# Kernel optimization log

Measured on AMD Instinct MI355X. Metric: run time of the kernel, lower is better.

Reference implementation:

```python
import jax, jax.numpy as jnp
import numpy as np
from jax import lax

B, T, N, F_IN = 4, 12, 2048, 26
HID, LF, FF, HOR, K = 128, 32, 256, 12, 2
E = 16384
N_TEMPORAL = 3
ALPHA, BETA = 0.9, 0.8   # synaptic / membrane decay constants
EPS = 1e-5
CH = [HID + LF, HID + 2 * LF]  # per-block channel sizes: 160, 192


def setup_inputs() -> dict:
    key = jax.random.key(0)
    ks = iter(jax.random.split(key, 64))
    def nrm(shape, s=0.02):
        return jax.random.normal(next(ks), shape, jnp.float32) * s
    inp = {
        "x": jax.random.normal(next(ks), (B, T, N, F_IN), jnp.float32),
        "edge_index": jax.random.randint(next(ks), (2, E), 0, N),
        "edge_weight": jax.random.uniform(next(ks), (E,), jnp.float32),
        "enc_w": nrm((F_IN, HID)), "enc_b": jnp.zeros((HID,), jnp.float32),
        "node_emb": nrm((N, HID)),
        "src_emb": nrm((N, HID), 0.1), "tgt_emb": nrm((N, HID), 0.1),
    }
    for i, c in enumerate(CH):
        inp[f"lw{i}"] = nrm((N, LF))
        inp[f"tW{i}"] = nrm((N_TEMPORAL, c, c))
        inp[f"tb{i}"] = jnp.zeros((N_TEMPORAL, c), jnp.float32)
        inp[f"dcw{i}"] = nrm((2 * K * c, c)); inp[f"dcb{i}"] = jnp.zeros((c,), jnp.float32)
        inp[f"dsw{i}"] = nrm((2 * c, c));     inp[f"dsb{i}"] = jnp.zeros((c,), jnp.float32)
        inp[f"skw{i}"] = nrm((c, FF));        inp[f"skb{i}"] = jnp.zeros((FF,), jnp.float32)
        inp[f"ng{i}"] = jnp.ones((c,), jnp.float32)
        inp[f"nb{i}"] = jnp.zeros((c,), jnp.float32)
    inp["rw1"] = nrm((FF, 2 * FF)); inp["rb1"] = jnp.zeros((2 * FF,), jnp.float32)
    inp["rw2"] = nrm((2 * FF, HOR * F_IN)); inp["rb2"] = jnp.zeros((HOR * F_IN,), jnp.float32)
    return inp


def _prop(x, s, d, w):
    """One diffusion step: gather x at source nodes, weight, scatter-add to dest. x:[b,t,n,c]."""
    m = x[:, :, s, :] * w[None, None, :, None]          # [b,t,E,c]
    m = jnp.moveaxis(m, 2, 0)                            # [E,b,t,c]
    y = jax.ops.segment_sum(m, d, num_segments=N)        # [n,b,t,c]
    return jnp.moveaxis(y, 0, 2)


def _synaptic_chain(h, Ws, bs):
    """n_layers of Linear + synaptic (2nd-order LIF) temporal recurrence; returns full sequence."""
    def step(carry, inp):
        syn, mem = carry
        syn = ALPHA * syn + inp
        mem = BETA * mem + syn
        return (syn, mem), mem
    for l in range(Ws.shape[0]):
        ht = jnp.moveaxis(h @ Ws[l] + bs[l], 1, 0)       # [t,b,n,c]
        z = jnp.zeros_like(ht[0])
        _, out = lax.scan(step, (z, z), ht)
        h = jnp.moveaxis(out, 0, 1)
    return h


def _diffconv(x, src, dst, ew, W, b):
    """Order-K diffusion conv over forward + backward transition matrices."""
    deg_f = jax.ops.segment_sum(ew, dst, num_segments=N)
    w_f = ew / jnp.clip(deg_f[dst], 1e-6)
    deg_b = jax.ops.segment_sum(ew, src, num_segments=N)
    w_b = ew / jnp.clip(deg_b[src], 1e-6)
    outs = []
    z = x
    for _ in range(K):
        z = _prop(z, src, dst, w_f); outs.append(z)
    z = x
    for _ in range(K):
        z = _prop(z, dst, src, w_b); outs.append(z)
    return jnp.concatenate(outs, -1) @ W + b


def _dense_conv(x, adj, W, b):
    """Dense graph conv order 2, include_self=False: concat[A x, A^2 x] -> Linear."""
    x1 = jnp.einsum('wv,btvc->btwc', adj, x)
    x2 = jnp.einsum('wv,btvc->btwc', adj, x1)
    return jnp.concatenate([x1, x2], -1) @ W + b


def _batch_norm(x, g, b):
    mu = x.mean((0, 1, 2))
    var = x.var((0, 1, 2))
    return (x - mu) / jnp.sqrt(var + EPS) * g + b


def reference(x, edge_index, edge_weight, enc_w, enc_b, node_emb, src_emb, tgt_emb,
              lw0, tW0, tb0, dcw0, dcb0, dsw0, dsb0, skw0, skb0, ng0, nb0,
              lw1, tW1, tb1, dcw1, dcb1, dsw1, dsb1, skw1, skb1, ng1, nb1,
              rw1, rb1, rw2, rb2):
    src, dst = edge_index[0], edge_index[1]
    h = x @ enc_w + enc_b + node_emb                     # encoder + node embedding
    adj = jax.nn.softmax(jax.nn.relu(src_emb @ tgt_emb.T), axis=1)  # learned adjacency
    out = jnp.zeros((1, h.shape[1], 1, 1), h.dtype)
    blocks = [(lw0, tW0, tb0, dcw0, dcb0, dsw0, dsb0, skw0, skb0, ng0, nb0),
              (lw1, tW1, tb1, dcw1, dcb1, dsw1, dsb1, skw1, skb1, ng1, nb1)]
    for (lw, tW, tb, dcw, dcb, dsw, dsb, skw, skb, ng, nb) in blocks:
        lwB = jnp.broadcast_to(lw, (h.shape[0], h.shape[1]) + lw.shape)
        h = jnp.concatenate([h, lwB], -1)                # LearnableWeight: append learned features
        res = h
        h = _synaptic_chain(h, tW, tb)                   # temporal chain (membrane potential)
        out = h @ skw + skb + out[:, -h.shape[1]:]       # skip connection accumulator
        xs = _diffconv(h, src, dst, edge_weight, dcw, dcb)
        h = xs + _dense_conv(h, adj, dsw, dsb)
        h = h + res[:, -h.shape[1]:]
        h = _batch_norm(h, ng, nb)
    r = jax.nn.relu(out[:, -1])                          # readout on last step: [B,N,FF]
    r = jax.nn.relu(r @ rw1 + rb1)
    y = r @ rw2 + rb2                                    # [B,N,HOR*F_IN]
    return y.reshape(B, N, HOR, F_IN).transpose(0, 2, 1, 3)  # [B,HOR,N,F_IN]
```

## Files before the change

### kernel.cpp

```cpp
#include <hip/hip_runtime.h>

using u16 = unsigned short;
typedef short bf16x8 __attribute__((ext_vector_type(8)));
typedef float f32x4  __attribute__((ext_vector_type(4)));

__device__ __forceinline__ float bf2f(u16 u) { return __uint_as_float(((unsigned)u) << 16); }
__device__ __forceinline__ u16 f2bf(float f) {
  unsigned u = __float_as_uint(f);
  return (u16)((u + 0x7FFFu + ((u >> 16) & 1u)) >> 16);
}
__device__ __forceinline__ float ldv(const float* p) { return *p; }
__device__ __forceinline__ float ldv(const u16* p)   { return bf2f(*p); }
__device__ __forceinline__ void  stv(float* p, float v) { *p = v; }
__device__ __forceinline__ void  stv(u16* p, float v)   { *p = f2bf(v); }

constexpr int cB = 4, cT = 12, cN = 2048, cF = 26;
constexpr int cHID = 128, cLF = 32, cFF = 256, cHOR = 12;
constexpr int cE = 16384;
constexpr int cR = cB * cT * cN;
constexpr int cBT = cB * cT;
constexpr float cALPHA = 0.9f, cBETA = 0.8f, cEPS = 1e-5f;

#define FLAG_ACC  1
#define FLAG_BIAS 2
#define FLAG_RELU 4

template <int NF, typename TC>
__global__ __launch_bounds__(256)
void gemm_mfma(const u16* __restrict__ A, const u16* __restrict__ BT,
               TC* __restrict__ C, const float* __restrict__ bias,
               int M, int N, int K, int lda, int ldbt, int ldc,
               long batchA, long batchB, long batchC, int flags, int biasPerT)
{
  constexpr int TN = NF * 32;
  constexpr int ROWS = 128 + TN;
  constexpr int NINST = ROWS / 16;
  constexpr int NPW = (NINST + 3) / 4;
  __shared__ __align__(16) u16 S[2][ROWS * 32];

  const long gx = gridDim.x, gy = gridDim.y;
  const long total = gx * gy * (long)gridDim.z;
  long lid = blockIdx.x + gx * (blockIdx.y + gy * (long)blockIdx.z);
  { const long q = total >> 3, r = total & 7, xcd = lid & 7, j = lid >> 3;
    lid = (xcd < r ? xcd * (q + 1) : r * (q + 1) + (xcd - r) * q) + j; }
  const int bz = (int)(lid / (gx * gy));
  const long rem = lid % (gx * gy);
  const int by = (int)(rem / gx), bx = (int)(rem % gx);

  A  += (long)bz * batchA;
  BT += (long)bz * batchB;
  C  += (long)bz * batchC;
  const int tid = threadIdx.x;
  const int lane = tid & 63, wid = tid >> 6;
  const int wm = wid & 1, wn = wid >> 1;
  const int m0 = bx * 128, n0 = by * TN;
  const int fr = lane & 15, kh = lane >> 4;
  const int nwi = (NINST - wid + 3) / 4;

  const u16* gp[NPW];
#pragma unroll
  for (int i = 0; i < NPW; ++i) {
    const int s = wid + i * 4;
    if (s < NINST) {
      const int slot = s * 64 + lane;
      const int row = slot >> 2, q = slot & 3;
      if (row < 128) {
        gp[i] = A + (long)(m0 + row) * lda + q * 8;
      } else {
        const int n = min(n0 + row - 128, N - 1);
        gp[i] = BT + (long)n * ldbt + q * 8;
      }
    } else {
      gp[i] = A;
    }
  }

  f32x4 acc[4][NF];
#pragma unroll
  for (int i = 0; i < 4; ++i)
#pragma unroll
    for (int j = 0; j < NF; ++j) acc[i][j] = f32x4{0.f, 0.f, 0.f, 0.f};

  auto STAGE = [&](int buf) {
#pragma unroll
    for (int i = 0; i < NPW; ++i) {
      if (i < nwi) {
        const int s = wid + i * 4;
        __builtin_amdgcn_global_load_lds(
            (const __attribute__((address_space(1))) unsigned int*)gp[i],
            (__attribute__((address_space(3))) unsigned int*)&S[buf][s * 512],
            16, 0, 0);
        gp[i] += 32;
      }
    }
  };

  STAGE(0);
  int cur = 0;
  for (int k0 = 0; k0 < K; k0 += 32) {
    __syncthreads();
    if (k0 + 32 < K) STAGE(cur ^ 1);
    bf16x8 af[4];
#pragma unroll
    for (int mf = 0; mf < 4; ++mf)
      af[mf] = *(const bf16x8*)&S[cur][(wm * 64 + mf * 16 + fr) * 32 + kh * 8];
#pragma unroll
    for (int nf = 0; nf < NF; ++nf) {
      const bf16x8 bfr =
          *(const bf16x8*)&S[cur][(128 + wn * NF * 16 + nf * 16 + fr) * 32 + kh * 8];
#pragma unroll
      for (int mf = 0; mf < 4; ++mf)
        acc[mf][nf] = __builtin_amdgcn_mfma_f32_16x16x32_bf16(af[mf], bfr, acc[mf][nf], 0, 0, 0);
    }
    cur ^= 1;
  }

  const float* bp = bias;
  if (biasPerT && bias) bp = bias + (long)((m0 >> 11) % cT) * N;

#pragma unroll
  for (int mf = 0; mf < 4; ++mf)
#pragma unroll
    for (int nf = 0; nf < NF; ++nf) {
      const int gn = n0 + wn * NF * 16 + nf * 16 + fr;
      if (gn < N) {
#pragma unroll
        for (int r = 0; r < 4; ++r) {
          const long gm = m0 + wm * 64 + mf * 16 + kh * 4 + r;
          float v = acc[mf][nf][r];
          if (flags & FLAG_BIAS) v += bp[gn];
          if (flags & FLAG_ACC)  v += ldv(&C[gm * ldc + gn]);
          if (flags & FLAG_RELU) v = fmaxf(v, 0.f);
          stv(&C[gm * ldc + gn], v);
        }
      }
    }
}

__global__ __launch_bounds__(256)
void matmul_small(const float* __restrict__ A, const float* __restrict__ B,
                  float* __restrict__ C, int M, int N, int K)
{
  const int idx = blockIdx.x * 256 + threadIdx.x;
  if (idx >= M * N) return;
  const int m = idx / N, n = idx % N;
  float acc = 0.f;
  for (int k = 0; k < K; ++k) acc = fmaf(A[m * K + k], B[k * N + n], acc);
  C[idx] = acc;
}

__device__ __forceinline__ void lif_coeffs(float* k1, float* k2, float* k3)
{
  float ap = 1.f;
  for (int m = 0; m < cT; ++m) {
    k1[m] = (m ? cBETA * k1[m - 1] : 0.f) + ap;
    ap *= cALPHA;
  }
  for (int m = 0; m < cT; ++m) { float s = 0.f; for (int i = 0; i <= m; ++i) s += k1[i] * k1[m - i]; k2[m] = s; }
  for (int m = 0; m < cT; ++m) { float s = 0.f; for (int i = 0; i <= m; ++i) s += k2[i] * k1[m - i]; k3[m] = s; }
}

__global__ void btot_full(const float* __restrict__ b1, const float* __restrict__ b2,
                          const float* __restrict__ b3, const float* __restrict__ W23,
                          const float* __restrict__ W3, float* __restrict__ Btot, int c)
{
  const int ch = threadIdx.x;
  if (ch >= c) return;
  float k1[cT], k2[cT], k3[cT]; lif_coeffs(k1, k2, k3);
  float v1 = 0.f, v2 = 0.f;
  for (int j = 0; j < c; ++j) { v1 = fmaf(b1[j], W23[j * c + ch], v1); v2 = fmaf(b2[j], W3[j * c + ch], v2); }
  float C1 = 0.f, C2 = 0.f, C3 = 0.f;
  for (int t = 0; t < cT; ++t) {
    C1 += k1[t]; C2 += k2[t]; C3 += k3[t];
    Btot[t * c + ch] = C3 * v1 + C2 * v2 + C1 * b3[ch];
  }
}

__global__ void btot_last(const float* __restrict__ b1, const float* __restrict__ b2,
                          const float* __restrict__ b3, const float* __restrict__ W23,
                          const float* __restrict__ W3, float* __restrict__ out, int c)
{
  const int ch = threadIdx.x;
  if (ch >= c) return;
  float k1[cT], k2[cT], k3[cT]; lif_coeffs(k1, k2, k3);
  float v1 = 0.f, v2 = 0.f;
  for (int j = 0; j < c; ++j) { v1 = fmaf(b1[j], W23[j * c + ch], v1); v2 = fmaf(b2[j], W3[j * c + ch], v2); }
  float C1 = 0.f, C2 = 0.f, C3 = 0.f;
  for (int t = 0; t < cT; ++t) { C1 += k1[t]; C2 += k2[t]; C3 += k3[t]; }
  out[ch] = C3 * v1 + C2 * v2 + C1 * b3[ch];
}

__global__ void bias_sk(const float* __restrict__ Btot11, const float* __restrict__ skw1,
                        const float* __restrict__ skb1, float* __restrict__ out)
{
  const int n = threadIdx.x;
  float acc = skb1[n];
  for (int k = 0; k < 192; ++k) acc = fmaf(Btot11[k], skw1[k * 256 + n], acc);
  out[n] = acc;
}

__global__ void vadd2(const float* __restrict__ a, const float* __restrict__ b,
                      float* __restrict__ o, int n)
{
  const int i = threadIdx.x;
  if (i < n) o[i] = a[i] + b[i];
}

__global__ __launch_bounds__(256)
void cascade3_full(const u16* __restrict__ in, u16* __restrict__ out, int c)
{
  const int c8 = c >> 3;
  const long total = (long)cB * cN * c8;
  const long idx = (long)blockIdx.x * 256 + threadIdx.x;
  if (idx >= total) return;
  const long nc = (long)cN * c;
  const int b = (int)(idx / ((long)cN * c8));
  const long rest = (idx % ((long)cN * c8)) * 8;
  const u16* p = in  + (long)b * cT * nc + rest;
  u16*       q = out + (long)b * cT * nc + rest;
  float s1[8] = {}, m1[8] = {}, s2[8] = {}, m2[8] = {}, s3[8] = {}, m3[8] = {};
#pragma unroll
  for (int t = 0; t < cT; ++t) {
    const bf16x8 v = *(const bf16x8*)&p[(long)t * nc];
    u16 o[8];
#pragma unroll
    for (int e = 0; e < 8; ++e) {
      s1[e] = fmaf(cALPHA, s1[e], bf2f((u16)v[e])); m1[e] = fmaf(cBETA, m1[e], s1[e]);
      s2[e] = fmaf(cALPHA, s2[e], m1[e]);           m2[e] = fmaf(cBETA, m2[e], s2[e]);
      s3[e] = fmaf(cALPHA, s3[e], m2[e]);           m3[e] = fmaf(cBETA, m3[e], s3[e]);
      o[e] = f2bf(m3[e]);
    }
    *(bf16x8*)&q[(long)t * nc] = *(const bf16x8*)o;
  }
}

__global__ __launch_bounds__(256)
void cascade3_last(const u16* __restrict__ in, u16* __restrict__ out, int c)
{
  const int c8 = c >> 3;
  const long total = (long)cB * cN * c8;
  const long idx = (long)blockIdx.x * 256 + threadIdx.x;
  if (idx >= total) return;
  const long nc = (long)cN * c;
  const int b = (int)(idx / ((long)cN * c8));
  const long rest = (idx % ((long)cN * c8)) * 8;
  const u16* p = in + (long)b * cT * nc + rest;
  float s1[8] = {}, m1[8] = {}, s2[8] = {}, m2[8] = {}, s3[8] = {}, m3[8] = {};
#pragma unroll
  for (int t = 0; t < cT; ++t) {
    const bf16x8 v = *(const bf16x8*)&p[(long)t * nc];
#pragma unroll
    for (int e = 0; e < 8; ++e) {
      s1[e] = fmaf(cALPHA, s1[e], bf2f((u16)v[e])); m1[e] = fmaf(cBETA, m1[e], s1[e]);
      s2[e] = fmaf(cALPHA, s2[e], m1[e]);           m2[e] = fmaf(cBETA, m2[e], s2[e]);
      s3[e] = fmaf(cALPHA, s3[e], m2[e]);           m3[e] = fmaf(cBETA, m3[e], s3[e]);
    }
  }
  u16 o[8];
#pragma unroll
  for (int e = 0; e < 8; ++e) o[e] = f2bf(m3[e]);
  *(bf16x8*)&out[(long)b * nc + rest] = *(const bf16x8*)o;
}

__global__ __launch_bounds__(256)
void wconvT(const float* __restrict__ w, u16* __restrict__ wt, int K, int N)
{
  const long idx = (long)blockIdx.x * 256 + threadIdx.x;
  if (idx >= (long)K * N) return;
  const int n = (int)(idx / K), k = (int)(idx % K);
  wt[idx] = f2bf(w[(long)k * N + n]);
}

__global__ __launch_bounds__(256)
void wconv_multi(const float* __restrict__ w0, u16* __restrict__ d0,
                 const float* __restrict__ w1, u16* __restrict__ d1,
                 const float* __restrict__ w2, u16* __restrict__ d2,
                 const float* __restrict__ w3, u16* __restrict__ d3,
                 const float* __restrict__ w4, u16* __restrict__ d4)
{
  const long s0 = 640L * 160, s1 = s0 + 320L * 160, s2 = s1 + 160L * 256,
             s3 = s2 + 256L * 512, s4 = s3 + 512L * 312;
  long idx = (long)blockIdx.x * 256 + threadIdx.x;
  const float* w; u16* d; int K, N; long base;
  if      (idx < s0) { w = w0; d = d0; K = 640; N = 160; base = 0;  }
  else if (idx < s1) { w = w1; d = d1; K = 320; N = 160; base = s0; }
  else if (idx < s2) { w = w2; d = d2; K = 160; N = 256; base = s1; }
  else if (idx < s3) { w = w3; d = d3; K = 256; N = 512; base = s2; }
  else if (idx < s4) { w = w4; d = d4; K = 512; N = 312; base = s3; }
  else return;
  const long l = idx - base;
  const int n = (int)(l / K), k = (int)(l % K);
  d[l] = f2bf(w[(long)k * N + n]);
}

__global__ __launch_bounds__(256)
void transpose_bf16(const u16* __restrict__ in, int ldi, u16* __restrict__ out,
                    int R, int Cc, long batchIn, long batchOut)
{
  __shared__ u16 t[64][65];
  in  += (long)blockIdx.z * batchIn;
  out += (long)blockIdx.z * batchOut;
  const int tid = threadIdx.x;
  const int r0 = blockIdx.x * 64, c0 = blockIdx.y * 64;
  for (int i = tid; i < 64 * 64; i += 256) {
    const int r = i >> 6, c = i & 63;
    t[r][c] = (r0 + r < R && c0 + c < Cc) ? in[(long)(r0 + r) * ldi + c0 + c] : (u16)0;
  }
  __syncthreads();
  for (int i = tid; i < 64 * 64; i += 256) {
    const int c = i >> 6, r = i & 63;
    if (c0 + c < Cc && r0 + r < R) out[(long)(c0 + c) * R + r0 + r] = t[r][c];
  }
}

__global__ __launch_bounds__(256)
void cvt_f2bf(const float* __restrict__ in, u16* __restrict__ out, long n)
{
  const long idx = (long)blockIdx.x * 256 + threadIdx.x;
  if (idx < n) out[idx] = f2bf(in[idx]);
}

__global__ __launch_bounds__(256)
void edge_stats(const int* __restrict__ s, const int* __restrict__ d,
                const float* __restrict__ ew, float* degf, float* degb,
                int* cntf, int* cntb)
{
  const int e = blockIdx.x * 256 + threadIdx.x;
  atomicAdd(&degf[d[e]], ew[e]);
  atomicAdd(&degb[s[e]], ew[e]);
  atomicAdd(&cntf[d[e]], 1);
  atomicAdd(&cntb[s[e]], 1);
}

__global__ __launch_bounds__(256)
void scan2(const int* __restrict__ cf, const int* __restrict__ cb,
           int* __restrict__ rf, int* __restrict__ rb)
{
  const int* c = blockIdx.x ? cb : cf;
  int* r       = blockIdx.x ? rb : rf;
  __shared__ int part[256];
  const int t = threadIdx.x, base = t * 8;
  int loc[8]; int s = 0;
#pragma unroll
  for (int i = 0; i < 8; ++i) { loc[i] = c[base + i]; s += loc[i]; }
  part[t] = s; __syncthreads();
  if (t == 0) {
    int run = 0;
    for (int i = 0; i < 256; ++i) { const int v = part[i]; part[i] = run; run += v; }
    r[2048] = run;
  }
  __syncthreads();
  int run = part[t];
#pragma unroll
  for (int i = 0; i < 8; ++i) { r[base + i] = run; run += loc[i]; }
}

__global__ __launch_bounds__(256)
void fill_csr(const int* __restrict__ s, const int* __restrict__ d,
              const float* __restrict__ ew,
              const float* __restrict__ degf, const float* __restrict__ degb,
              const int* __restrict__ rowf, const int* __restrict__ rowb,
              int* curf, int* curb,
              int* __restrict__ colf, int* __restrict__ colb,
              float* __restrict__ wnf, float* __restrict__ wnb)
{
  const int e = blockIdx.x * 256 + threadIdx.x;
  const int si = s[e], di = d[e];
  const float w = ew[e];
  const int p = rowf[di] + atomicAdd(&curf[di], 1);
  colf[p] = si; wnf[p] = w / fmaxf(degf[di], 1e-6f);
  const int q = rowb[si] + atomicAdd(&curb[si], 1);
  colb[q] = di; wnb[q] = w / fmaxf(degb[si], 1e-6f);
}

constexpr int cNPB = 12;
constexpr int cNCH = (cN + cNPB - 1) / cNPB;
__global__ __launch_bounds__(256)
void prop_gather_bt(const u16* __restrict__ x, int ldx, u16* __restrict__ y, int ldy,
                    const int* __restrict__ rowptr, const int* __restrict__ col,
                    const float* __restrict__ w)
{
  const int lid = blockIdx.x;
  const int xcd = lid & 7, j = lid >> 3;
  const int bt = xcd * 6 + (j % 6);
  const int chunk = j / 6;
  const int item = threadIdx.x;
  if (item >= cNPB * 20) return;
  const int n = chunk * cNPB + item / 20;
  if (n >= cN) return;
  const int ch = (item % 20) * 8;
  const int beg = rowptr[n], end = rowptr[n + 1];
  const u16* xb = x + (long)bt * cN * ldx + ch;
  float acc[8] = {};
  int jj = beg;
  for (; jj + 1 < end; jj += 2) {
    const int c0 = col[jj], c1 = col[jj + 1];
    const float w0 = w[jj], w1 = w[jj + 1];
    const bf16x8 v0 = *(const bf16x8*)&xb[(long)c0 * ldx];
    const bf16x8 v1 = *(const bf16x8*)&xb[(long)c1 * ldx];
#pragma unroll
    for (int q = 0; q < 8; ++q) {
      acc[q] = fmaf(w0, bf2f((u16)v0[q]), acc[q]);
      acc[q] = fmaf(w1, bf2f((u16)v1[q]), acc[q]);
    }
  }
  if (jj < end) {
    const float w0 = w[jj];
    const bf16x8 v0 = *(const bf16x8*)&xb[(long)col[jj] * ldx];
#pragma unroll
    for (int q = 0; q < 8; ++q) acc[q] = fmaf(w0, bf2f((u16)v0[q]), acc[q]);
  }
  u16 o[8];
#pragma unroll
  for (int q = 0; q < 8; ++q) o[q] = f2bf(acc[q]);
  *(bf16x8*)&y[((long)bt * cN + n) * ldy + ch] = *(const bf16x8*)o;
}

__global__ __launch_bounds__(160)
void encoder(const float* __restrict__ x, const float* __restrict__ ew_,
             const float* __restrict__ eb, const float* __restrict__ ne,
             const float* __restrict__ lw, u16* __restrict__ h)
{
  __shared__ float xs[cF];
  const int tid = threadIdx.x;
  const long r0 = (long)blockIdx.x * 8;
  for (long row = r0; row < r0 + 8; ++row) {
    if (tid < cF) xs[tid] = x[row * cF + tid];
    __syncthreads();
    const int n = (int)(row % cN);
    float v;
    if (tid < cHID) {
      float acc = eb[tid] + ne[(long)n * cHID + tid];
#pragma unroll
      for (int f = 0; f < cF; ++f) acc = fmaf(xs[f], ew_[f * cHID + tid], acc);
      v = acc;
    } else {
      v = lw[(long)n * cLF + (tid - cHID)];
    }
    h[row * 160 + tid] = f2bf(v);
    __syncthreads();
  }
}

__global__ __launch_bounds__(256)
void relu_softmax_rows(const float* __restrict__ sc, u16* __restrict__ adj)
{
  const int row = blockIdx.x, tid = threadIdx.x;
  const float* p = sc + (long)row * cN;
  __shared__ float red[256];
  float lv[8];
  float mx = 0.f;
#pragma unroll
  for (int i = 0; i < 8; ++i) {
    const float v = fmaxf(p[tid + i * 256], 0.f);
    lv[i] = v; mx = fmaxf(mx, v);
  }
  red[tid] = mx; __syncthreads();
  for (int s = 128; s > 0; s >>= 1) { if (tid < s) red[tid] = fmaxf(red[tid], red[tid + s]); __syncthreads(); }
  const float m = red[0]; __syncthreads();
  float sum = 0.f;
#pragma unroll
  for (int i = 0; i < 8; ++i) { lv[i] = __expf(lv[i] - m); sum += lv[i]; }
  red[tid] = sum; __syncthreads();
  for (int s = 128; s > 0; s >>= 1) { if (tid < s) red[tid] += red[tid + s]; __syncthreads(); }
  const float inv = 1.f / red[0]; __syncthreads();
#pragma unroll
  for (int i = 0; i < 8; ++i) adj[(long)row * cN + tid + i * 256] = f2bf(lv[i] * inv);
}

__global__ __launch_bounds__(256)
void bn_stats(const u16* __restrict__ d, const u16* __restrict__ res,
              float* __restrict__ stat, int c)
{
  const int ch = threadIdx.x;
  const long r0 = (long)blockIdx.x * (cR / 512);
  float s = 0.f, s2 = 0.f;
  for (int i = 0; i < cR / 512; ++i) {
    const float v = bf2f(d[(r0 + i) * c + ch]) + bf2f(res[(r0 + i) * c + ch]);
    s += v; s2 = fmaf(v, v, s2);
  }
  atomicAdd(&stat[ch], s);
  atomicAdd(&stat[c + ch], s2);
}

__global__ __launch_bounds__(256)
void bn_finalize(const float* __restrict__ stat, const float* __restrict__ g,
                 const float* __restrict__ b, float* __restrict__ scsh, int c)
{
  const int ch = threadIdx.x;
  const float mu = stat[ch] / cR;
  const float var = stat[c + ch] / cR - mu * mu;
  const float sc = g[ch] * rsqrtf(var + cEPS);
  scsh[ch] = sc;
  scsh[c + ch] = fmaf(-mu, sc, b[ch]);
}

__global__ __launch_bounds__(192)
void bn_apply_concat(const u16* __restrict__ d, const u16* __restrict__ res,
                     const float* __restrict__ scsh, const float* __restrict__ lw,
                     u16* __restrict__ out)
{
  const int tid = threadIdx.x;
  const long r0 = (long)blockIdx.x * 8;
  for (long row = r0; row < r0 + 8; ++row) {
    const int n = (int)(row % cN);
    float v;
    if (tid < 160) v = fmaf(bf2f(d[row * 160 + tid]) + bf2f(res[row * 160 + tid]),
                            scsh[tid], scsh[160 + tid]);
    else           v = lw[(long)n * cLF + (tid - 160)];
    out[row * 192 + tid] = f2bf(v);
  }
}

__global__ __launch_bounds__(256)
void final_transpose(const float* __restrict__ y, float* __restrict__ out)
{
  const long idx = (long)blockIdx.x * 256 + threadIdx.x;
  const int f = (int)(idx % cF);
  long t = idx / cF;
  const int n = (int)(t % cN); t /= cN;
  const int hor = (int)(t % cHOR);
  const int b = (int)(t / cHOR);
  out[idx] = y[((long)b * cN + n) * (cHOR * cF) + hor * cF + f];
}

__global__ __launch_bounds__(256)
void fill_f32(float* __restrict__ out, long n, float val)
{
  const long idx = (long)blockIdx.x * 256 + threadIdx.x;
  if (idx < n) out[idx] = val;
}

extern "C" void kernel_launch(void* const* d_in, const int* in_sizes, int n_in,
                              void* d_out, int out_size, void* d_ws, size_t ws_size,
                              hipStream_t stream)
{
  float* outF = (float*)d_out;
  const long outN = out_size;
  if (n_in < 34) { fill_f32<<<(int)((outN + 255) / 256), 256, 0, stream>>>(outF, outN, 500.f); return; }
  if (in_sizes[0] != cB * cT * cN * cF || in_sizes[1] != 2 * cE || in_sizes[9] != 3 * 160 * 160) {
    fill_f32<<<(int)((outN + 255) / 256), 256, 0, stream>>>(outF, outN, 700.f); return;
  }

  const float* x        = (const float*)d_in[0];
  const int*   eidx     = (const int*)d_in[1];
  const float* ew       = (const float*)d_in[2];
  const float* enc_w    = (const float*)d_in[3];
  const float* enc_b    = (const float*)d_in[4];
  const float* node_emb = (const float*)d_in[5];
  const float* src_emb  = (const float*)d_in[6];
  const float* tgt_emb  = (const float*)d_in[7];
  const float* lw0  = (const float*)d_in[8];
  const float* tW0  = (const float*)d_in[9];
  const float* tb0  = (const float*)d_in[10];
  const float* dcw0 = (const float*)d_in[11];
  const float* dcb0 = (const float*)d_in[12];
  const float* dsw0 = (const float*)d_in[13];
  const float* dsb0 = (const float*)d_in[14];
  const float* skw0 = (const float*)d_in[15];
  const float* skb0 = (const float*)d_in[16];
  const float* ng0  = (const float*)d_in[17];
  const float* nb0  = (const float*)d_in[18];
  const float* lw1  = (const float*)d_in[19];
  const float* tW1  = (const float*)d_in[20];
  const float* tb1  = (const float*)d_in[21];
  const float* skw1 = (const float*)d_in[26];
  const float* skb1 = (const float*)d_in[27];
  const float* rw1  = (const float*)d_in[30];
  const float* rb1  = (const float*)d_in[31];
  const float* rw2  = (const float*)d_in[32];
  const float* rb2  = (const float*)d_in[33];
  const int* srcI = eidx;
  const int* dstI = eidx + cE;

  char* W = (char*)d_ws;
  size_t off = 0;
  auto A8 = [&](size_t bytes) { size_t r = off; off = (off + bytes + 255) & ~(size_t)255; return r; };
  const size_t oH0 = A8((size_t)cR * 160 * 2);
  const size_t oHh = A8((size_t)cR * 160 * 2);
  const size_t oT1 = A8((size_t)cR * 160 * 2);
  const size_t oS2 = A8((size_t)cR * 160 * 2);
  const size_t oDd = A8((size_t)cR * 160 * 2);
  const size_t oAdj = A8((size_t)cN * cN * 2);
  const size_t oOut = A8((size_t)cB * cN * cFF * 4);
  const size_t oR1  = A8((size_t)cB * cN * 512 * 2);
  const size_t oY   = A8((size_t)cB * cN * cHOR * cF * 4);
  const size_t oZero = A8(6 * 2048 * 4 + 2 * 192 * 4);
  const size_t oRowf = A8(2049 * 4), oRowb = A8(2049 * 4);
  const size_t oColf = A8((size_t)cE * 4), oColb = A8((size_t)cE * 4);
  const size_t oWnf  = A8((size_t)cE * 4), oWnb  = A8((size_t)cE * 4);
  const size_t oScSh = A8(2 * 192 * 4);
  const size_t oWT   = A8((size_t)721920 * 2);
  const size_t oSeb  = A8((size_t)cN * cHID * 2);
  const size_t oTeb  = A8((size_t)cN * cHID * 2);
  const size_t oW23  = A8(192 * 192 * 4);
  const size_t oW123 = A8(192 * 192 * 4);
  const size_t oWskp = A8(192 * 256 * 4);
  const size_t oBt0  = A8(cT * 160 * 4);
  const size_t oBt11 = A8(192 * 4);
  const size_t oBsk1 = A8(256 * 4);
  const size_t oBsum = A8(160 * 4);
  if (off > ws_size) {
    fill_f32<<<(int)((outN + 255) / 256), 256, 0, stream>>>(outF, outN, 300.f);
    return;
  }

  u16 *H0 = (u16*)(W + oH0), *Hh = (u16*)(W + oHh), *T1 = (u16*)(W + oT1),
      *S2 = (u16*)(W + oS2), *adjb = (u16*)(W + oAdj);
  u16* Dd = (u16*)(W + oDd);
  u16 *G1 = (u16*)(W + oHh);
  u16 *Z12 = T1;
  float* scores = (float*)(W + oDd);
  float *outacc = (float*)(W + oOut), *yb = (float*)(W + oY);
  u16 *r1b = (u16*)(W + oR1);
  float* zero = (float*)(W + oZero);
  float *degf = zero, *degb = zero + 2048;
  int *cntf = (int*)(zero + 4096), *cntb = cntf + 2048,
      *curf = cntb + 2048, *curb = curf + 2048;
  float* stat = (float*)(curb + 2048);
  int *rowf = (int*)(W + oRowf), *rowb = (int*)(W + oRowb);
  int *colf = (int*)(W + oColf), *colb = (int*)(W + oColb);
  float *wnf = (float*)(W + oWnf), *wnb = (float*)(W + oWnb);
  float* scsh = (float*)(W + oScSh);
  u16* wt   = (u16*)(W + oWT);
  u16 *wt123_0 = wt,            *wsk1pT = wt + 3 * 25600, *wdc = wsk1pT + 3 * 36864,
      *wds = wdc + 102400,      *wsk0 = wds + 51200,
      *wr1 = wsk0 + 40960 + 49152, *wr2 = wr1 + 131072;
  u16 *seb = (u16*)(W + oSeb), *teb = (u16*)(W + oTeb);
  float *W23 = (float*)(W + oW23), *W123 = (float*)(W + oW123), *Wskp = (float*)(W + oWskp);
  float *Bt0 = (float*)(W + oBt0), *Bt11 = (float*)(W + oBt11), *Bsk1 = (float*)(W + oBsk1);
  float *Bsum = (float*)(W + oBsum);

  auto g5u = [&](const u16* Aq, const u16* Bq, u16* Cq, const float* bias,
                 int M, int N, int K, int lda, int ldbt, int ldc,
                 long bA, long bB, long bC, int batch, int flags, int bpt = 0) {
    dim3 g(M / 128, (N + 159) / 160, batch);
    gemm_mfma<5, u16><<<g, 256, 0, stream>>>(Aq, Bq, Cq, bias, M, N, K, lda, ldbt, ldc, bA, bB, bC, flags, bpt);
  };
  auto g4f = [&](const u16* Aq, const u16* Bq, float* Cq, const float* bias,
                 int M, int N, int K, int lda, int ldbt, int ldc,
                 long bA, long bB, long bC, int batch, int flags) {
    dim3 g(M / 128, (N + 127) / 128, batch);
    gemm_mfma<4, float><<<g, 256, 0, stream>>>(Aq, Bq, Cq, bias, M, N, K, lda, ldbt, ldc, bA, bB, bC, flags, 0);
  };
  auto g4u = [&](const u16* Aq, const u16* Bq, u16* Cq, const float* bias,
                 int M, int N, int K, int lda, int ldbt, int ldc, int flags) {
    dim3 g(M / 128, (N + 127) / 128, 1);
    gemm_mfma<4, u16><<<g, 256, 0, stream>>>(Aq, Bq, Cq, bias, M, N, K, lda, ldbt, ldc, 0, 0, 0, flags, 0);
  };
  auto wcv = [&](const float* src, u16* dst, int K, int N) {
    wconvT<<<(int)(((long)K * N + 255) / 256), 256, 0, stream>>>(src, dst, K, N);
  };
  auto mms = [&](const float* Aq, const float* Bq, float* Cq, int M, int N, int K) {
    matmul_small<<<(M * N + 255) / 256, 256, 0, stream>>>(Aq, Bq, Cq, M, N, K);
  };

  mms(tW0 + 1L * 25600, tW0 + 2L * 25600, W23, 160, 160, 160);
  mms(tW0,              W23,              W123, 160, 160, 160);
  wcv(W123, wt123_0, 160, 160);
  btot_full<<<1, 160, 0, stream>>>(tb0, tb0 + 160, tb0 + 320, W23, tW0 + 2L * 25600, Bt0, 160);
  mms(tW1 + 1L * 36864, tW1 + 2L * 36864, W23, 192, 192, 192);
  mms(tW1,              W23,              W123, 192, 192, 192);
  mms(W123, skw1, Wskp, 192, 256, 192);
  wcv(Wskp, wsk1pT, 192, 256);
  btot_last<<<1, 192, 0, stream>>>(tb1, tb1 + 192, tb1 + 384, W23, tW1 + 2L * 36864, Bt11, 192);
  bias_sk<<<1, 256, 0, stream>>>(Bt11, skw1, skb1, Bsk1);
  vadd2<<<1, 160, 0, stream>>>(dcb0, dsb0, Bsum, 160);

  {
    const long tot = 640L * 160 + 320L * 160 + 160L * 256 + 256L * 512 + 512L * 312;
    wconv_multi<<<(int)((tot + 255) / 256), 256, 0, stream>>>(
        dcw0, wdc, dsw0, wds, skw0, wsk0, rw1, wr1, rw2, wr2);
  }
  hipMemsetAsync(zero, 0, 6 * 2048 * 4 + 2 * 192 * 4, stream);
  edge_stats<<<cE / 256, 256, 0, stream>>>(srcI, dstI, ew, degf, degb, cntf, cntb);
  scan2<<<2, 256, 0, stream>>>(cntf, cntb, rowf, rowb);
  fill_csr<<<cE / 256, 256, 0, stream>>>(srcI, dstI, ew, degf, degb, rowf, rowb,
                                         curf, curb, colf, colb, wnf, wnb);
  encoder<<<cR / 8, 160, 0, stream>>>(x, enc_w, enc_b, node_emb, lw0, H0);

  cvt_f2bf<<<(cN * cHID + 255) / 256, 256, 0, stream>>>(src_emb, seb, (long)cN * cHID);
  cvt_f2bf<<<(cN * cHID + 255) / 256, 256, 0, stream>>>(tgt_emb, teb, (long)cN * cHID);
  g4f(seb, teb, scores, nullptr, cN, cN, cHID, cHID, cHID, cN, 0, 0, 0, 1, 0);
  relu_softmax_rows<<<cN, 256, 0, stream>>>(scores, adjb);

  const int PROP_GRID = 8 * 6 * cNCH;

  {
    const int c = 160;
    const long NC = (long)cN * c;
    const int casGrid = (int)(((long)cB * cN * (c / 8) + 255) / 256);
    cascade3_full<<<casGrid, 256, 0, stream>>>(H0, T1, c);
    g5u(T1, wt123_0, Hh, Bt0, cR, c, c, c, c, c, 0, 0, 0, 1, FLAG_BIAS, 1);
    g4f(Hh + 11L * NC, wsk0, outacc, skb0, cN, cFF, c, c, c, cFF,
        (long)cT * NC, 0, (long)cN * cFF, cB, FLAG_BIAS);
    dim3 tg(cN / 64, (c + 63) / 64, cBT);
    transpose_bf16<<<tg, 256, 0, stream>>>(Hh, c, S2, cN, c, NC, NC);
    g5u(adjb, S2, T1, nullptr, cN, c, cN, cN, cN, c, 0, NC, NC, cBT, 0);
    g5u(T1, wds, Dd, Bsum, cR, c, c, c, 320, c, 0, 0, 0, 1, FLAG_BIAS);
    transpose_bf16<<<tg, 256, 0, stream>>>(T1, c, S2, cN, c, NC, NC);
    g5u(adjb, S2, T1, nullptr, cN, c, cN, cN, cN, c, 0, NC, NC, cBT, 0);
    g5u(T1, wds + 160, Dd, nullptr, cR, c, c, c, 320, c, 0, 0, 0, 1, FLAG_ACC);
    prop_gather_bt<<<PROP_GRID, 256, 0, stream>>>(Hh, 160, Z12, 320, rowf, colf, wnf);
    prop_gather_bt<<<PROP_GRID, 256, 0, stream>>>(Z12, 320, Z12 + 160, 320, rowf, colf, wnf);
    g5u(Z12, wdc, Dd, nullptr, cR, c, 320, 320, 640, c, 0, 0, 0, 1, FLAG_ACC);
    prop_gather_bt<<<PROP_GRID, 256, 0, stream>>>(Hh, 160, Z12, 320, rowb, colb, wnb);
    prop_gather_bt<<<PROP_GRID, 256, 0, stream>>>(Z12, 320, Z12 + 160, 320, rowb, colb, wnb);
    g5u(Z12, wdc + 320, Dd, nullptr, cR, c, 320, 320, 640, c, 0, 0, 0, 1, FLAG_ACC);
    bn_stats<<<512, c, 0, stream>>>(Dd, H0, stat, c);
    bn_finalize<<<1, c, 0, stream>>>(stat, ng0, nb0, scsh, c);
    bn_apply_concat<<<cR / 8, 192, 0, stream>>>(Dd, H0, scsh, lw1, G1);
  }

  {
    const int c = 192;
    const int casGrid = (int)(((long)cB * cN * (c / 8) + 255) / 256);
    cascade3_last<<<casGrid, 256, 0, stream>>>(G1, S2, c);
    g4f(S2, wsk1pT, outacc, Bsk1, cB * cN, cFF, c, c, c, cFF,
        0, 0, 0, 1, FLAG_BIAS | FLAG_ACC | FLAG_RELU);
  }

  cvt_f2bf<<<(int)(((long)cB * cN * cFF + 255) / 256), 256, 0, stream>>>(outacc, S2, (long)cB * cN * cFF);
  g4u(S2, wr1, r1b, rb1, cB * cN, 2 * cFF, cFF, cFF, cFF, 2 * cFF, FLAG_BIAS | FLAG_RELU);
  g4f(r1b, wr2, yb, rb2, cB * cN, cHOR * cF, 2 * cFF, 2 * cFF, 2 * cFF, cHOR * cF,
      0, 0, 0, 1, FLAG_BIAS);
  final_transpose<<<(cB * cHOR * cN * cF) / 256, 256, 0, stream>>>(yb, outF);
}
```

Baseline: 1.173 ms.

## Pack diffusion and dense-conv operands into one K=480 GEMM per direction

The two diffusion hops and the dense adjacency matmul output are now written into one packed [R,480] buffer per direction. A single GEMM against packed dcw/dsw weights replaces the four separate K=160/320 GEMMs, which cuts GEMM launches and the repeated read-modify-write of the accumulator. The skip accumulator, the readout hidden layer and the readout output are now kept in bf16, which removes a separate convert kernel and halves that traffic but adds rounding error. The two embedding conversions are merged into one launch.

```diff
diff --git a/kernel.cpp b/kernel.cpp
--- a/kernel.cpp
+++ b/kernel.cpp
@@ -272,19 +272,29 @@
 }
 
 __global__ __launch_bounds__(256)
-void wconv_multi(const float* __restrict__ w0, u16* __restrict__ d0,
-                 const float* __restrict__ w1, u16* __restrict__ d1,
-                 const float* __restrict__ w2, u16* __restrict__ d2,
+void wpack_dcds(const float* __restrict__ dcw, const float* __restrict__ dsw,
+                u16* __restrict__ W1, u16* __restrict__ W2)
+{
+  const int idx = blockIdx.x * 256 + threadIdx.x;
+  if (idx >= 2 * 160 * 480) return;
+  const int which = idx / (160 * 480);
+  const int l = idx % (160 * 480);
+  const int n = l / 480, k = l % 480;
+  float v;
+  if (k < 320) v = dcw[(long)(which * 320 + k) * 160 + n];
+  else         v = dsw[(long)(which * 160 + (k - 320)) * 160 + n];
+  (which ? W2 : W1)[l] = f2bf(v);
+}
+
+__global__ __launch_bounds__(256)
+void wconv_multi(const float* __restrict__ w2, u16* __restrict__ d2,
                  const float* __restrict__ w3, u16* __restrict__ d3,
                  const float* __restrict__ w4, u16* __restrict__ d4)
 {
-  const long s0 = 640L * 160, s1 = s0 + 320L * 160, s2 = s1 + 160L * 256,
-             s3 = s2 + 256L * 512, s4 = s3 + 512L * 312;
+  const long s2 = 160L * 256, s3 = s2 + 256L * 512, s4 = s3 + 512L * 312;
   long idx = (long)blockIdx.x * 256 + threadIdx.x;
   const float* w; u16* d; int K, N; long base;
-  if      (idx < s0) { w = w0; d = d0; K = 640; N = 160; base = 0;  }
-  else if (idx < s1) { w = w1; d = d1; K = 320; N = 160; base = s0; }
-  else if (idx < s2) { w = w2; d = d2; K = 160; N = 256; base = s1; }
+  if      (idx < s2) { w = w2; d = d2; K = 160; N = 256; base = 0;  }
   else if (idx < s3) { w = w3; d = d3; K = 256; N = 512; base = s2; }
   else if (idx < s4) { w = w4; d = d4; K = 512; N = 312; base = s3; }
   else return;
@@ -314,10 +324,12 @@
 }
 
 __global__ __launch_bounds__(256)
-void cvt_f2bf(const float* __restrict__ in, u16* __restrict__ out, long n)
+void cvt2_f2bf(const float* __restrict__ a, u16* __restrict__ oa,
+               const float* __restrict__ b, u16* __restrict__ ob, long n)
 {
   const long idx = (long)blockIdx.x * 256 + threadIdx.x;
-  if (idx < n) out[idx] = f2bf(in[idx]);
+  if (idx < n) oa[idx] = f2bf(a[idx]);
+  else if (idx < 2 * n) ob[idx - n] = f2bf(b[idx - n]);
 }
 
 __global__ __launch_bounds__(256)
@@ -513,7 +525,7 @@
 }
 
 __global__ __launch_bounds__(256)
-void final_transpose(const float* __restrict__ y, float* __restrict__ out)
+void final_transpose(const u16* __restrict__ y, float* __restrict__ out)
 {
   const long idx = (long)blockIdx.x * 256 + threadIdx.x;
   const int f = (int)(idx % cF);
@@ -521,7 +533,7 @@
   const int n = (int)(t % cN); t /= cN;
   const int hor = (int)(t % cHOR);
   const int b = (int)(t / cHOR);
-  out[idx] = y[((long)b * cN + n) * (cHOR * cF) + hor * cF + f];
+  out[idx] = bf2f(y[((long)b * cN + n) * (cHOR * cF) + hor * cF + f]);
 }
 
 __global__ __launch_bounds__(256)
@@ -578,19 +590,17 @@
   auto A8 = [&](size_t bytes) { size_t r = off; off = (off + bytes + 255) & ~(size_t)255; return r; };
   const size_t oH0 = A8((size_t)cR * 160 * 2);
   const size_t oHh = A8((size_t)cR * 160 * 2);
-  const size_t oT1 = A8((size_t)cR * 160 * 2);
-  const size_t oS2 = A8((size_t)cR * 160 * 2);
+  const size_t oPK = A8((size_t)cR * 480 * 2);
+  const size_t oSx = A8((size_t)cR * 160 * 2);
   const size_t oDd = A8((size_t)cR * 160 * 2);
   const size_t oAdj = A8((size_t)cN * cN * 2);
-  const size_t oOut = A8((size_t)cB * cN * cFF * 4);
-  const size_t oR1  = A8((size_t)cB * cN * 512 * 2);
-  const size_t oY   = A8((size_t)cB * cN * cHOR * cF * 4);
+  const size_t oOut = A8((size_t)cB * cN * cFF * 2);
   const size_t oZero = A8(6 * 2048 * 4 + 2 * 192 * 4);
   const size_t oRowf = A8(2049 * 4), oRowb = A8(2049 * 4);
   const size_t oColf = A8((size_t)cE * 4), oColb = A8((size_t)cE * 4);
   const size_t oWnf  = A8((size_t)cE * 4), oWnb  = A8((size_t)cE * 4);
   const size_t oScSh = A8(2 * 192 * 4);
-  const size_t oWT   = A8((size_t)721920 * 2);
+  const size_t oWT   = A8((size_t)600000 * 2);
   const size_t oSeb  = A8((size_t)cN * cHID * 2);
   const size_t oTeb  = A8((size_t)cN * cHID * 2);
   const size_t oW23  = A8(192 * 192 * 4);
@@ -605,14 +615,13 @@
     return;
   }
 
-  u16 *H0 = (u16*)(W + oH0), *Hh = (u16*)(W + oHh), *T1 = (u16*)(W + oT1),
-      *S2 = (u16*)(W + oS2), *adjb = (u16*)(W + oAdj);
-  u16* Dd = (u16*)(W + oDd);
-  u16 *G1 = (u16*)(W + oHh);
-  u16 *Z12 = T1;
-  float* scores = (float*)(W + oDd);
-  float *outacc = (float*)(W + oOut), *yb = (float*)(W + oY);
-  u16 *r1b = (u16*)(W + oR1);
+  u16 *H0 = (u16*)(W + oH0), *Hh = (u16*)(W + oHh), *PK = (u16*)(W + oPK),
+      *Sx = (u16*)(W + oSx), *Dd = (u16*)(W + oDd), *adjb = (u16*)(W + oAdj);
+  u16 *G1 = Hh;
+  float* scores = (float*)PK;
+  u16 *r1b = PK + 16L * 1024 * 1024;
+  u16 *ybB = PK + 28L * 1024 * 1024;
+  u16 *outB = (u16*)(W + oOut);
   float* zero = (float*)(W + oZero);
   float *degf = zero, *degb = zero + 2048;
   int *cntf = (int*)(zero + 4096), *cntb = cntf + 2048,
@@ -622,10 +631,11 @@
   int *colf = (int*)(W + oColf), *colb = (int*)(W + oColb);
   float *wnf = (float*)(W + oWnf), *wnb = (float*)(W + oWnb);
   float* scsh = (float*)(W + oScSh);
-  u16* wt   = (u16*)(W + oWT);
-  u16 *wt123_0 = wt,            *wsk1pT = wt + 3 * 25600, *wdc = wsk1pT + 3 * 36864,
-      *wds = wdc + 102400,      *wsk0 = wds + 51200,
-      *wr1 = wsk0 + 40960 + 49152, *wr2 = wr1 + 131072;
+  u16* wt = (u16*)(W + oWT);
+  u16 *wt123_0 = wt,               *wsk1pT = wt123_0 + 25600,
+      *W1pk = wsk1pT + 49152,      *W2pk = W1pk + 76800,
+      *wsk0 = W2pk + 76800,        *wr1 = wsk0 + 40960,
+      *wr2 = wr1 + 131072;
   u16 *seb = (u16*)(W + oSeb), *teb = (u16*)(W + oTeb);
   float *W23 = (float*)(W + oW23), *W123 = (float*)(W + oW123), *Wskp = (float*)(W + oWskp);
   float *Bt0 = (float*)(W + oBt0), *Bt11 = (float*)(W + oBt11), *Bsk1 = (float*)(W + oBsk1);
@@ -644,9 +654,10 @@
     gemm_mfma<4, float><<<g, 256, 0, stream>>>(Aq, Bq, Cq, bias, M, N, K, lda, ldbt, ldc, bA, bB, bC, flags, 0);
   };
   auto g4u = [&](const u16* Aq, const u16* Bq, u16* Cq, const float* bias,
-                 int M, int N, int K, int lda, int ldbt, int ldc, int flags) {
-    dim3 g(M / 128, (N + 127) / 128, 1);
-    gemm_mfma<4, u16><<<g, 256, 0, stream>>>(Aq, Bq, Cq, bias, M, N, K, lda, ldbt, ldc, 0, 0, 0, flags, 0);
+                 int M, int N, int K, int lda, int ldbt, int ldc,
+                 long bA, long bB, long bC, int batch, int flags) {
+    dim3 g(M / 128, (N + 127) / 128, batch);
+    gemm_mfma<4, u16><<<g, 256, 0, stream>>>(Aq, Bq, Cq, bias, M, N, K, lda, ldbt, ldc, bA, bB, bC, flags, 0);
   };
   auto wcv = [&](const float* src, u16* dst, int K, int N) {
     wconvT<<<(int)(((long)K * N + 255) / 256), 256, 0, stream>>>(src, dst, K, N);
@@ -667,10 +678,10 @@
   bias_sk<<<1, 256, 0, stream>>>(Bt11, skw1, skb1, Bsk1);
   vadd2<<<1, 160, 0, stream>>>(dcb0, dsb0, Bsum, 160);
 
+  wpack_dcds<<<(2 * 160 * 480 + 255) / 256, 256, 0, stream>>>(dcw0, dsw0, W1pk, W2pk);
   {
-    const long tot = 640L * 160 + 320L * 160 + 160L * 256 + 256L * 512 + 512L * 312;
-    wconv_multi<<<(int)((tot + 255) / 256), 256, 0, stream>>>(
-        dcw0, wdc, dsw0, wds, skw0, wsk0, rw1, wr1, rw2, wr2);
+    const long tot = 160L * 256 + 256L * 512 + 512L * 312;
+    wconv_multi<<<(int)((tot + 255) / 256), 256, 0, stream>>>(skw0, wsk0, rw1, wr1, rw2, wr2);
   }
   hipMemsetAsync(zero, 0, 6 * 2048 * 4 + 2 * 192 * 4, stream);
   edge_stats<<<cE / 256, 256, 0, stream>>>(srcI, dstI, ew, degf, degb, cntf, cntb);
@@ -679,8 +690,7 @@
                                          curf, curb, colf, colb, wnf, wnb);
   encoder<<<cR / 8, 160, 0, stream>>>(x, enc_w, enc_b, node_emb, lw0, H0);
 
-  cvt_f2bf<<<(cN * cHID + 255) / 256, 256, 0, stream>>>(src_emb, seb, (long)cN * cHID);
-  cvt_f2bf<<<(cN * cHID + 255) / 256, 256, 0, stream>>>(tgt_emb, teb, (long)cN * cHID);
+  cvt2_f2bf<<<(2 * cN * cHID + 255) / 256, 256, 0, stream>>>(src_emb, seb, tgt_emb, teb, (long)cN * cHID);
   g4f(seb, teb, scores, nullptr, cN, cN, cHID, cHID, cHID, cN, 0, 0, 0, 1, 0);
   relu_softmax_rows<<<cN, 256, 0, stream>>>(scores, adjb);
 
@@ -689,24 +699,23 @@
   {
     const int c = 160;
     const long NC = (long)cN * c;
+    const long PB = (long)cN * 480;
     const int casGrid = (int)(((long)cB * cN * (c / 8) + 255) / 256);
-    cascade3_full<<<casGrid, 256, 0, stream>>>(H0, T1, c);
-    g5u(T1, wt123_0, Hh, Bt0, cR, c, c, c, c, c, 0, 0, 0, 1, FLAG_BIAS, 1);
-    g4f(Hh + 11L * NC, wsk0, outacc, skb0, cN, cFF, c, c, c, cFF,
+    cascade3_full<<<casGrid, 256, 0, stream>>>(H0, Sx, c);
+    g5u(Sx, wt123_0, Hh, Bt0, cR, c, c, c, c, c, 0, 0, 0, 1, FLAG_BIAS, 1);
+    g4u(Hh + 11L * NC, wsk0, outB, skb0, cN, cFF, c, c, c, cFF,
         (long)cT * NC, 0, (long)cN * cFF, cB, FLAG_BIAS);
     dim3 tg(cN / 64, (c + 63) / 64, cBT);
-    transpose_bf16<<<tg, 256, 0, stream>>>(Hh, c, S2, cN, c, NC, NC);
-    g5u(adjb, S2, T1, nullptr, cN, c, cN, cN, cN, c, 0, NC, NC, cBT, 0);
-    g5u(T1, wds, Dd, Bsum, cR, c, c, c, 320, c, 0, 0, 0, 1, FLAG_BIAS);
-    transpose_bf16<<<tg, 256, 0, stream>>>(T1, c, S2, cN, c, NC, NC);
-    g5u(adjb, S2, T1, nullptr, cN, c, cN, cN, cN, c, 0, NC, NC, cBT, 0);
-    g5u(T1, wds + 160, Dd, nullptr, cR, c, c, c, 320, c, 0, 0, 0, 1, FLAG_ACC);
-    prop_gather_bt<<<PROP_GRID, 256, 0, stream>>>(Hh, 160, Z12, 320, rowf, colf, wnf);
-    prop_gather_bt<<<PROP_GRID, 256, 0, stream>>>(Z12, 320, Z12 + 160, 320, rowf, colf, wnf);
-    g5u(Z12, wdc, Dd, nullptr, cR, c, 320, 320, 640, c, 0, 0, 0, 1, FLAG_ACC);
-    prop_gather_bt<<<PROP_GRID, 256, 0, stream>>>(Hh, 160, Z12, 320, rowb, colb, wnb);
-    prop_gather_bt<<<PROP_GRID, 256, 0, stream>>>(Z12, 320, Z12 + 160, 320, rowb, colb, wnb);
-    g5u(Z12, wdc + 320, Dd, nullptr, cR, c, 320, 320, 640, c, 0, 0, 0, 1, FLAG_ACC);
+    transpose_bf16<<<tg, 256, 0, stream>>>(Hh, c, Sx, cN, c, NC, NC);
+    prop_gather_bt<<<PROP_GRID, 256, 0, stream>>>(Hh, 160, PK, 480, rowf, colf, wnf);
+    prop_gather_bt<<<PROP_GRID, 256, 0, stream>>>(PK, 480, PK + 160, 480, rowf, colf, wnf);
+    g5u(adjb, Sx, PK + 320, nullptr, cN, c, cN, cN, cN, 480, 0, NC, PB, cBT, 0);
+    g5u(PK, W1pk, Dd, Bsum, cR, c, 480, 480, 480, c, 0, 0, 0, 1, FLAG_BIAS);
+    transpose_bf16<<<tg, 256, 0, stream>>>(PK + 320, 480, Sx, cN, c, PB, NC);
+    prop_gather_bt<<<PROP_GRID, 256, 0, stream>>>(Hh, 160, PK, 480, rowb, colb, wnb);
+    prop_gather_bt<<<PROP_GRID, 256, 0, stream>>>(PK, 480, PK + 160, 480, rowb, colb, wnb);
+    g5u(adjb, Sx, PK + 320, nullptr, cN, c, cN, cN, cN, 480, 0, NC, PB, cBT, 0);
+    g5u(PK, W2pk, Dd, nullptr, cR, c, 480, 480, 480, c, 0, 0, 0, 1, FLAG_ACC);
     bn_stats<<<512, c, 0, stream>>>(Dd, H0, stat, c);
     bn_finalize<<<1, c, 0, stream>>>(stat, ng0, nb0, scsh, c);
     bn_apply_concat<<<cR / 8, 192, 0, stream>>>(Dd, H0, scsh, lw1, G1);
@@ -715,14 +724,14 @@
   {
     const int c = 192;
     const int casGrid = (int)(((long)cB * cN * (c / 8) + 255) / 256);
-    cascade3_last<<<casGrid, 256, 0, stream>>>(G1, S2, c);
-    g4f(S2, wsk1pT, outacc, Bsk1, cB * cN, cFF, c, c, c, cFF,
+    cascade3_last<<<casGrid, 256, 0, stream>>>(G1, Sx, c);
+    g4u(Sx, wsk1pT, outB, Bsk1, cB * cN, cFF, c, c, c, cFF,
         0, 0, 0, 1, FLAG_BIAS | FLAG_ACC | FLAG_RELU);
   }
 
-  cvt_f2bf<<<(int)(((long)cB * cN * cFF + 255) / 256), 256, 0, stream>>>(outacc, S2, (long)cB * cN * cFF);
-  g4u(S2, wr1, r1b, rb1, cB * cN, 2 * cFF, cFF, cFF, cFF, 2 * cFF, FLAG_BIAS | FLAG_RELU);
-  g4f(r1b, wr2, yb, rb2, cB * cN, cHOR * cF, 2 * cFF, 2 * cFF, 2 * cFF, cHOR * cF,
+  g4u(outB, wr1, r1b, rb1, cB * cN, 2 * cFF, cFF, cFF, cFF, 2 * cFF,
+      0, 0, 0, 1, FLAG_BIAS | FLAG_RELU);
+  g4u(r1b, wr2, ybB, rb2, cB * cN, cHOR * cF, 2 * cFF, 2 * cFF, 2 * cFF, cHOR * cF,
       0, 0, 0, 1, FLAG_BIAS);
-  final_transpose<<<(cB * cHOR * cN * cF) / 256, 256, 0, stream>>>(yb, outF);
-}
+  final_transpose<<<(cB * cHOR * cN * cF) / 256, 256, 0, stream>>>(ybB, outF);
+}
```

New measurement: 1.099 ms. -6.3%, faster.
